# Performance work log

Hardware: AMD Instinct MI355X
Metric: run time of the kernel (lower is better)

## Reference

```python
import jax, jax.numpy as jnp
import numpy as np

HIDDEN = 2048
NUM_HEADS = 8
NUM_KV_HEADS = 1
HEAD_DIM = 256
ROPE_THETA = 10000.0
B, S = 2, 2048


def setup_inputs() -> dict:
    key = jax.random.key(0)
    k1, k2, k3, k4, k5 = jax.random.split(key, 5)
    scale = 0.02
    hidden_states = jax.random.normal(k1, (B, S, HIDDEN), dtype=jnp.float32)
    Wq = jax.random.normal(k2, (HIDDEN, NUM_HEADS * HEAD_DIM), dtype=jnp.float32) * scale
    Wk = jax.random.normal(k3, (HIDDEN, NUM_KV_HEADS * HEAD_DIM), dtype=jnp.float32) * scale
    Wv = jax.random.normal(k4, (HIDDEN, NUM_KV_HEADS * HEAD_DIM), dtype=jnp.float32) * scale
    Wo = jax.random.normal(k5, (NUM_HEADS * HEAD_DIM, HIDDEN), dtype=jnp.float32) * scale
    # causal mask: 1 = attend, 0 = masked (module adds -1e9 where mask==0)
    attention_mask = jnp.tril(jnp.ones((S, S), dtype=jnp.int32))[None, None].repeat(B, axis=0)
    position_ids = jnp.arange(S, dtype=jnp.int32)[None, :].repeat(B, axis=0)
    return {"hidden_states": hidden_states, "Wq": Wq, "Wk": Wk, "Wv": Wv,
            "Wo": Wo, "attention_mask": attention_mask, "position_ids": position_ids}


def _rotate_half(x):
    half = x.shape[-1] // 2
    return jnp.concatenate([-x[..., half:], x[..., :half]], axis=-1)


def _rope_cos_sin(position_ids, head_dim, theta):
    inv_freq = 1.0 / (theta ** (jnp.arange(0, head_dim, 2, dtype=jnp.float32) / head_dim))
    freqs = position_ids.astype(jnp.float32)[:, :, None] * inv_freq[None, None, :]  # [B,S,D/2]
    emb = jnp.concatenate([freqs, freqs], axis=-1)  # [B,S,D]
    return jnp.cos(emb)[:, None], jnp.sin(emb)[:, None]  # [B,1,S,D]


def reference(hidden_states, Wq, Wk, Wv, Wo, attention_mask, position_ids):
    bsz, q_len, _ = hidden_states.shape
    q = (hidden_states @ Wq).reshape(bsz, q_len, NUM_HEADS, HEAD_DIM).transpose(0, 2, 1, 3)
    k = (hidden_states @ Wk).reshape(bsz, q_len, NUM_KV_HEADS, HEAD_DIM).transpose(0, 2, 1, 3)
    v = (hidden_states @ Wv).reshape(bsz, q_len, NUM_KV_HEADS, HEAD_DIM).transpose(0, 2, 1, 3)
    q = q / jnp.sqrt(jnp.float32(HEAD_DIM))  # scale before RoPE, as in source
    cos, sin = _rope_cos_sin(position_ids, HEAD_DIM, ROPE_THETA)
    q = q * cos + _rotate_half(q) * sin
    k = k * cos + _rotate_half(k) * sin
    # GQA: repeat kv heads (prefill: cache == current k,v)
    groups = NUM_HEADS // NUM_KV_HEADS
    k = jnp.repeat(k, groups, axis=1)
    v = jnp.repeat(v, groups, axis=1)
    attn = jnp.einsum('bhqd,bhkd->bhqk', q, k)  # [B,H,S,S]
    additive = jnp.where(attention_mask == 0, jnp.float32(-1e9), jnp.float32(0.0))
    attn = jax.nn.softmax(attn + additive, axis=-1)
    out = jnp.einsum('bhqk,bhkd->bhqd', attn, v)
    out = out.transpose(0, 2, 1, 3).reshape(bsz, q_len, NUM_HEADS * HEAD_DIM)
    out = out @ Wo
    return out, attn
```

## Files before the change

kernel.cpp:

```cpp
#include <hip/hip_runtime.h>

typedef __bf16 bf16_t;
typedef __attribute__((ext_vector_type(4))) float f32x4;
typedef __attribute__((ext_vector_type(8))) __bf16 bf16x8;
typedef __attribute__((ext_vector_type(4))) __bf16 bf16x4;

#define DEVI __device__ __forceinline__

static constexpr int kBsz = 2, kS = 2048, kH = 8, kD = 256, kHid = 2048, kNqkv = 2560;

DEVI void gload_lds16(const void* g, void* l) {
  __builtin_amdgcn_global_load_lds(
      (__attribute__((address_space(1))) unsigned int*)g,
      (__attribute__((address_space(3))) unsigned int*)l, 16, 0, 0);
}

__global__ __launch_bounds__(256) void cast_f32_bf16(const float* __restrict__ in,
                                                     bf16_t* __restrict__ out) {
  int idx = blockIdx.x * 256 + threadIdx.x;
  const float4 f = ((const float4*)in)[idx];
  bf16x4 o;
  o[0] = (bf16_t)f.x; o[1] = (bf16_t)f.y; o[2] = (bf16_t)f.z; o[3] = (bf16_t)f.w;
  ((bf16x4*)out)[idx] = o;
}

__global__ __launch_bounds__(256) void zero_f32(float* __restrict__ p) {
  p[blockIdx.x * 256 + threadIdx.x] = 0.f;
}

__global__ void wtrans_all(const float* __restrict__ Wq, const float* __restrict__ Wk,
                           const float* __restrict__ Wv, const float* __restrict__ Wo,
                           bf16_t* __restrict__ WqkvT, bf16_t* __restrict__ WoT) {
  __shared__ float tile[32][33];
  int zb = blockIdx.x;
  const float* src;
  bf16_t* dst;
  int C, bx, by;
  if (zb < 4096) {
    src = Wq; dst = WqkvT; C = 2048; bx = zb & 63; by = zb >> 6;
  } else if (zb < 4608) {
    int u = zb - 4096; src = Wk; dst = WqkvT + (size_t)2048 * 2048; C = 256; bx = u & 7; by = u >> 3;
  } else if (zb < 5120) {
    int u = zb - 4608; src = Wv; dst = WqkvT + (size_t)2304 * 2048; C = 256; bx = u & 7; by = u >> 3;
  } else {
    int u = zb - 5120; src = Wo; dst = WoT; C = 2048; bx = u & 63; by = u >> 6;
  }
  int c0 = bx * 32, r0 = by * 32;
  int tx = threadIdx.x, ty = threadIdx.y;
#pragma unroll
  for (int k = 0; k < 4; k++)
    tile[ty + 8 * k][tx] = src[(size_t)(r0 + ty + 8 * k) * C + c0 + tx];
  __syncthreads();
#pragma unroll
  for (int k = 0; k < 4; k++)
    dst[(size_t)(c0 + ty + 8 * k) * 2048 + r0 + tx] = (bf16_t)tile[tx][ty + 8 * k];
}

__global__ __launch_bounds__(256) void transpose_v(const bf16_t* __restrict__ qkv,
                                                   bf16_t* __restrict__ vT) {
  __shared__ float tile[32][33];
  int d0 = blockIdx.x * 32, s0 = blockIdx.y * 32, b = blockIdx.z;
  int tx = threadIdx.x, ty = threadIdx.y;
  const bf16_t* in = qkv + ((size_t)(b * kS + s0)) * kNqkv + 2304 + d0;
#pragma unroll
  for (int k = 0; k < 4; k++)
    tile[ty + 8 * k][tx] = (float)in[(size_t)(ty + 8 * k) * kNqkv + tx];
  __syncthreads();
  bf16_t* out = vT + ((size_t)(b * kD + d0)) * kS + s0;
#pragma unroll
  for (int k = 0; k < 4; k++)
    out[(size_t)(ty + 8 * k) * kS + tx] = (bf16_t)tile[tx][ty + 8 * k];
}

__global__ __launch_bounds__(256) void rope_all(const bf16_t* __restrict__ qkv,
                                                const int* __restrict__ pos_ids,
                                                bf16_t* __restrict__ q_bh,
                                                bf16_t* __restrict__ k_b) {
  int bid = blockIdx.x;
  if (bid < 16384) {
    int idx = bid * 256 + threadIdx.x;
    int j = idx & 127, s = (idx >> 7) & 2047, h = (idx >> 18) & 7, b = idx >> 21;
    float invf = exp2f(-0.103810253f * (float)j);
    float ang = (float)pos_ids[b * kS + s] * invf;
    float c, sn;
    sincosf(ang, &sn, &c);
    const bf16_t* src = qkv + ((size_t)(b * kS + s)) * kNqkv + h * kD;
    float x0 = (float)src[j] * 0.0625f;
    float x1 = (float)src[j + 128] * 0.0625f;
    bf16_t* dst = q_bh + ((size_t)((b * kH + h) * kS + s)) * kD;
    dst[j] = (bf16_t)(x0 * c - x1 * sn);
    dst[j + 128] = (bf16_t)(x1 * c + x0 * sn);
  } else {
    int idx = (bid - 16384) * 256 + threadIdx.x;
    int j = idx & 127, s = (idx >> 7) & 2047, b = idx >> 18;
    float invf = exp2f(-0.103810253f * (float)j);
    float ang = (float)pos_ids[b * kS + s] * invf;
    float c, sn;
    sincosf(ang, &sn, &c);
    const bf16_t* src = qkv + ((size_t)(b * kS + s)) * kNqkv + 2048;
    float x0 = (float)src[j];
    float x1 = (float)src[j + 128];
    bf16_t* dst = k_b + ((size_t)(b * kS + s)) * kD;
    dst[j] = (bf16_t)(x0 * c - x1 * sn);
    dst[j + 128] = (bf16_t)(x1 * c + x0 * sn);
  }
}

__global__ __launch_bounds__(256, 4) void qk_exp(
    const bf16_t* __restrict__ q_bh, const bf16_t* __restrict__ k_b,
    bf16_t* __restrict__ P, float* __restrict__ rowsum) {
  __shared__ bf16_t ks[64 * 256];
  const int u = blockIdx.x;
  const int z = blockIdx.y;
  const int b = z >> 3;
  int rt = (int)((sqrtf(8.f * (float)u + 1.f) - 1.f) * 0.5f);
  while ((rt + 1) * (rt + 2) / 2 <= u) rt++;
  while (rt * (rt + 1) / 2 > u) rt--;
  const int kt = u - rt * (rt + 1) / 2;
  const int m0 = rt * 64, n0 = kt * 64;
  const int t = threadIdx.x, lane = t & 63, wv = t >> 6;
  const int wm2 = (wv & 1) * 32, wn2 = (wv >> 1) * 32;
  const int lrow = lane & 15, quad = lane >> 4;

  const bf16_t* kb = k_b + (size_t)b * kS * kD;
#pragma unroll
  for (int i = 0; i < 8; i++) {
    int slot = i * 256 + t;
    int r = slot >> 5;
    int c = (slot & 31) ^ (r & 7);
    gload_lds16(kb + (size_t)(n0 + r) * kD + c * 8, ks + slot * 8);
  }
  bf16x8 qf[2][8];
  {
    const bf16_t* qb = q_bh + ((size_t)z * kS + m0) * kD;
#pragma unroll
    for (int mi = 0; mi < 2; mi++)
#pragma unroll
      for (int k8 = 0; k8 < 8; k8++)
        qf[mi][k8] = *(const bf16x8*)(qb + (size_t)(wm2 + mi * 16 + lrow) * kD + k8 * 32 + quad * 8);
  }
  __syncthreads();

  f32x4 acc[2][2];
#pragma unroll
  for (int mi = 0; mi < 2; mi++)
#pragma unroll
    for (int ni = 0; ni < 2; ni++) acc[mi][ni] = f32x4{0.f, 0.f, 0.f, 0.f};
  __builtin_amdgcn_s_setprio(1);
#pragma unroll
  for (int k8 = 0; k8 < 8; k8++) {
    bf16x8 bfv[2];
#pragma unroll
    for (int ni = 0; ni < 2; ni++) {
      int R = wn2 + ni * 16 + lrow;
      int c16 = (k8 * 4 + quad) ^ (R & 7);
      bfv[ni] = *(const bf16x8*)(ks + R * 256 + c16 * 8);
    }
#pragma unroll
    for (int mi = 0; mi < 2; mi++)
#pragma unroll
      for (int ni = 0; ni < 2; ni++)
        acc[mi][ni] = __builtin_amdgcn_mfma_f32_16x16x32_bf16(qf[mi][k8], bfv[ni], acc[mi][ni], 0, 0, 0);
  }
  __builtin_amdgcn_s_setprio(0);

  const bool diag = (kt == rt);
  bf16_t* pt = P + ((size_t)z * kS + m0) * kS + n0;
#pragma unroll
  for (int mi = 0; mi < 2; mi++)
#pragma unroll
    for (int rr = 0; rr < 4; rr++) {
      int ml = wm2 + mi * 16 + quad * 4 + rr;
      int mg = m0 + ml;
      float s4 = 0.f;
#pragma unroll
      for (int ni = 0; ni < 2; ni++) {
        int nl = wn2 + ni * 16 + lrow;
        int ng = n0 + nl;
        float e = __expf(fminf(acc[mi][ni][rr], 80.f));
        bool ok = !diag || ng <= mg;
        bf16_t pb = ok ? (bf16_t)e : (bf16_t)0.f;
        pt[(size_t)ml * kS + nl] = pb;
        s4 += (float)pb;
      }
      s4 += __shfl_xor(s4, 1); s4 += __shfl_xor(s4, 2);
      s4 += __shfl_xor(s4, 4); s4 += __shfl_xor(s4, 8);
      if (lrow == 0) atomicAdd(rowsum + (size_t)z * kS + mg, s4);
    }

  if (diag && !(rt & 1)) {
    bf16x8 zz = {(bf16_t)0.f, (bf16_t)0.f, (bf16_t)0.f, (bf16_t)0.f,
                 (bf16_t)0.f, (bf16_t)0.f, (bf16_t)0.f, (bf16_t)0.f};
    int r = t >> 2, cc = (t & 3) * 16;
    bf16_t* pz = P + ((size_t)z * kS + m0 + r) * kS + n0 + 64 + cc;
    *(bf16x8*)pz = zz;
    *(bf16x8*)(pz + 8) = zz;
  }
}

__global__ __launch_bounds__(256) void attn_expand(
    const bf16_t* __restrict__ P, const float* __restrict__ rowsum,
    float* __restrict__ attn) {
  const int rt = blockIdx.y, z = blockIdx.z;
  const int m0 = rt * 64;
  const int t = threadIdx.x;
  const int r = t >> 2;
  const int cbase = blockIdx.x * 512 + (t & 3) * 8;
  const int ncaus = (rt + 1) * 64;
  const float inv = 1.f / rowsum[(size_t)z * kS + m0 + r];
  const size_t rowoff = ((size_t)z * kS + m0 + r) * kS;
  const bf16_t* pr = P + rowoff;
  float* ar = attn + rowoff;
#pragma unroll
  for (int it = 0; it < 16; it++) {
    int col = cbase + it * 32;
    float4 o0, o1;
    if (col < ncaus) {
      bf16x8 pv = *(const bf16x8*)(pr + col);
      o0 = make_float4((float)pv[0] * inv, (float)pv[1] * inv,
                       (float)pv[2] * inv, (float)pv[3] * inv);
      o1 = make_float4((float)pv[4] * inv, (float)pv[5] * inv,
                       (float)pv[6] * inv, (float)pv[7] * inv);
    } else {
      o0 = make_float4(0.f, 0.f, 0.f, 0.f);
      o1 = o0;
    }
    *(float4*)(ar + col) = o0;
    *(float4*)(ar + col + 4) = o1;
  }
}

template <int OUT, int CKTR, int BAL = 0>
__global__ __launch_bounds__(256) void gemm_bt(
    const bf16_t* __restrict__ Av, const bf16_t* __restrict__ Btv, void* __restrict__ Cv,
    int K, int lda, int ldb, int ldc,
    long long aBatch, long long bBatch, int bzShift, long long cBatch,
    const float* __restrict__ rowsum) {
  constexpr int BM = 128, BN = 128, BK = 64;
  __shared__ bf16_t As[BM * BK];
  __shared__ bf16_t Bs[BN * BK];
  const int z = blockIdx.z;
  const int n0 = blockIdx.x * BN;
  int byi = blockIdx.y;
  if (BAL) {
    if ((blockIdx.x ^ (blockIdx.z >> 3)) & 1) byi = gridDim.y - 1 - byi;
  }
  const int m0 = byi * BM;
  const bf16_t* Bt = Btv + (size_t)(z >> bzShift) * bBatch + (size_t)n0 * ldb;
  const int kEnd = CKTR ? ((m0 + BM < K) ? (m0 + BM) : K) : K;
  const int t = threadIdx.x;
  const int lane = t & 63, wv = t >> 6;
  const int wm = (wv & 1) << 6, wn = (wv >> 1) << 6;
  const int lrow = lane & 15, quad = lane >> 4;
  f32x4 zero = {0.f, 0.f, 0.f, 0.f};
  f32x4 acc[4][4];
#pragma unroll
  for (int i = 0; i < 4; i++)
#pragma unroll
    for (int j = 0; j < 4; j++) acc[i][j] = zero;

  const bf16_t* Ab = Av + (size_t)z * aBatch + (size_t)m0 * lda;

  for (int k0 = 0; k0 < kEnd; k0 += BK) {
    __syncthreads();
#pragma unroll
    for (int i = 0; i < 4; i++) {
      int slot = i * 256 + t;
      int r = slot >> 3, c = slot & 7;
      gload_lds16(Ab + (size_t)r * lda + k0 + c * 8, As + slot * 8);
    }
#pragma unroll
    for (int i = 0; i < 4; i++) {
      int slot = i * 256 + t;
      int r = slot >> 3, c = slot & 7;
      gload_lds16(Bt + (size_t)r * ldb + k0 + c * 8, Bs + slot * 8);
    }
    __syncthreads();
#pragma unroll
    for (int k8 = 0; k8 < 2; k8++) {
      bf16x8 af[4], bfv[4];
#pragma unroll
      for (int i = 0; i < 4; i++)
        af[i] = *(const bf16x8*)(As + (wm + i * 16 + lrow) * BK + k8 * 32 + quad * 8);
#pragma unroll
      for (int i = 0; i < 4; i++)
        bfv[i] = *(const bf16x8*)(Bs + (wn + i * 16 + lrow) * BK + k8 * 32 + quad * 8);
#pragma unroll
      for (int mi = 0; mi < 4; mi++)
#pragma unroll
        for (int ni = 0; ni < 4; ni++)
          acc[mi][ni] = __builtin_amdgcn_mfma_f32_16x16x32_bf16(af[mi], bfv[ni], acc[mi][ni], 0, 0, 0);
    }
  }

  if (OUT == 0) {
    float* C = (float*)Cv + (size_t)z * cBatch;
#pragma unroll
    for (int mi = 0; mi < 4; mi++) {
      int m = m0 + wm + mi * 16 + quad * 4;
#pragma unroll
      for (int ni = 0; ni < 4; ni++) {
        int n = n0 + wn + ni * 16 + lrow;
#pragma unroll
        for (int r = 0; r < 4; r++) C[(size_t)(m + r) * ldc + n] = acc[mi][ni][r];
      }
    }
  } else if (OUT == 1) {
    bf16_t* C = (bf16_t*)Cv + (size_t)(z >> 3) * cBatch + (size_t)(z & 7) * kD;
#pragma unroll
    for (int mi = 0; mi < 4; mi++) {
      int m = m0 + wm + mi * 16 + quad * 4;
      float inv[4];
#pragma unroll
      for (int r = 0; r < 4; r++) inv[r] = 1.f / rowsum[(size_t)z * kS + m + r];
#pragma unroll
      for (int ni = 0; ni < 4; ni++) {
        int n = n0 + wn + ni * 16 + lrow;
#pragma unroll
        for (int r = 0; r < 4; r++)
          C[(size_t)(m + r) * ldc + n] = (bf16_t)(acc[mi][ni][r] * inv[r]);
      }
    }
  } else {
    bf16_t* C = (bf16_t*)Cv + (size_t)z * cBatch;
#pragma unroll
    for (int mi = 0; mi < 4; mi++) {
      int m = m0 + wm + mi * 16 + quad * 4;
#pragma unroll
      for (int ni = 0; ni < 4; ni++) {
        int n = n0 + wn + ni * 16 + lrow;
#pragma unroll
        for (int r = 0; r < 4; r++) C[(size_t)(m + r) * ldc + n] = (bf16_t)acc[mi][ni][r];
      }
    }
  }
}

extern "C" void kernel_launch(void* const* d_in, const int* in_sizes, int n_in,
                              void* d_out, int out_size, void* d_ws, size_t ws_size,
                              hipStream_t stream) {
  const float* hs = (const float*)d_in[0];
  const float* Wq = (const float*)d_in[1];
  const float* Wk = (const float*)d_in[2];
  const float* Wv = (const float*)d_in[3];
  const float* Wo = (const float*)d_in[4];
  const int* pos = (const int*)d_in[6];

  float* out = (float*)d_out;
  float* attn = out + (size_t)kBsz * kS * kHid;

  char* w = (char*)d_ws;
  bf16_t* hsb = (bf16_t*)w;   w += (size_t)4096 * 2048 * 2;
  bf16_t* WqkvT = (bf16_t*)w; w += (size_t)2560 * 2048 * 2;
  bf16_t* WoT = (bf16_t*)w;   w += (size_t)2048 * 2048 * 2;
  bf16_t* qkv = (bf16_t*)w;   w += (size_t)4096 * 2560 * 2;
  bf16_t* q_bh = (bf16_t*)w;  w += (size_t)8388608 * 2;
  bf16_t* k_b = (bf16_t*)w;   w += (size_t)1048576 * 2;
  bf16_t* vT = (bf16_t*)w;    w += (size_t)1048576 * 2;
  bf16_t* av = (bf16_t*)w;    w += (size_t)8388608 * 2;
  bf16_t* Pb = (bf16_t*)w;    w += (size_t)16 * 2048 * 2048 * 2;
  float* rowsum = (float*)w;  w += (size_t)16 * 2048 * 4;

  cast_f32_bf16<<<8192, 256, 0, stream>>>(hs, hsb);
  wtrans_all<<<9216, dim3(32, 8), 0, stream>>>(Wq, Wk, Wv, Wo, WqkvT, WoT);
  zero_f32<<<128, 256, 0, stream>>>(rowsum);

  gemm_bt<2, 0><<<dim3(20, 32, 1), 256, 0, stream>>>(
      hsb, WqkvT, qkv, 2048, 2048, 2048, 2560, 0, 0, 0, 0, nullptr);

  rope_all<<<18432, 256, 0, stream>>>(qkv, pos, q_bh, k_b);
  transpose_v<<<dim3(8, 64, 2), dim3(32, 8), 0, stream>>>(qkv, vT);

  qk_exp<<<dim3(528, 16), 256, 0, stream>>>(q_bh, k_b, Pb, rowsum);

  attn_expand<<<dim3(4, 32, 16), 256, 0, stream>>>(Pb, rowsum, attn);

  gemm_bt<1, 1, 1><<<dim3(2, 16, 16), 256, 0, stream>>>(
      Pb, vT, av, 2048, 2048, 2048, 2048,
      (long long)4194304, (long long)524288, 3, (long long)(kS * kHid), rowsum);

  gemm_bt<0, 0><<<dim3(16, 32, 1), 256, 0, stream>>>(
      av, WoT, out, 2048, 2048, 2048, 2048, 0, 0, 0, 0, nullptr);
}
```

Baseline: 740.3 us.

## Merge prep and rope/transpose kernels; stage bf16 GEMM epilogue through LDS

Combines the cast, weight-transpose and rowsum-zero kernels into one launch, and the RoPE and V-transpose kernels into another, reducing launch count. The bf16-output GEMM epilogues now write the tile into swizzled shared memory and then emit coalesced 16-byte row stores instead of scattered 2-byte stores. This adds an extra LDS round trip and two barriers per tile, and puts divergent block roles in the merged kernels.

```diff
diff --git a/kernel.cpp b/kernel.cpp
--- a/kernel.cpp
+++ b/kernel.cpp
@@ -15,38 +15,42 @@
       (__attribute__((address_space(3))) unsigned int*)l, 16, 0, 0);
 }
 
-__global__ __launch_bounds__(256) void cast_f32_bf16(const float* __restrict__ in,
-                                                     bf16_t* __restrict__ out) {
-  int idx = blockIdx.x * 256 + threadIdx.x;
-  const float4 f = ((const float4*)in)[idx];
-  bf16x4 o;
-  o[0] = (bf16_t)f.x; o[1] = (bf16_t)f.y; o[2] = (bf16_t)f.z; o[3] = (bf16_t)f.w;
-  ((bf16x4*)out)[idx] = o;
-}
-
-__global__ __launch_bounds__(256) void zero_f32(float* __restrict__ p) {
-  p[blockIdx.x * 256 + threadIdx.x] = 0.f;
-}
-
-__global__ void wtrans_all(const float* __restrict__ Wq, const float* __restrict__ Wk,
-                           const float* __restrict__ Wv, const float* __restrict__ Wo,
-                           bf16_t* __restrict__ WqkvT, bf16_t* __restrict__ WoT) {
+__global__ __launch_bounds__(256) void prep_all(
+    const float* __restrict__ hs, const float* __restrict__ Wq,
+    const float* __restrict__ Wk, const float* __restrict__ Wv,
+    const float* __restrict__ Wo, bf16_t* __restrict__ hsb,
+    bf16_t* __restrict__ WqkvT, bf16_t* __restrict__ WoT,
+    float* __restrict__ rowsum) {
   __shared__ float tile[32][33];
-  int zb = blockIdx.x;
+  const int zb = blockIdx.x;
+  const int t = threadIdx.x;
+  if (zb < 8192) {
+    int idx = zb * 256 + t;
+    const float4 f = ((const float4*)hs)[idx];
+    bf16x4 o;
+    o[0] = (bf16_t)f.x; o[1] = (bf16_t)f.y; o[2] = (bf16_t)f.z; o[3] = (bf16_t)f.w;
+    ((bf16x4*)hsb)[idx] = o;
+    return;
+  }
+  if (zb >= 17408) {
+    rowsum[(zb - 17408) * 256 + t] = 0.f;
+    return;
+  }
+  const int u = zb - 8192;
   const float* src;
   bf16_t* dst;
   int C, bx, by;
-  if (zb < 4096) {
-    src = Wq; dst = WqkvT; C = 2048; bx = zb & 63; by = zb >> 6;
-  } else if (zb < 4608) {
-    int u = zb - 4096; src = Wk; dst = WqkvT + (size_t)2048 * 2048; C = 256; bx = u & 7; by = u >> 3;
-  } else if (zb < 5120) {
-    int u = zb - 4608; src = Wv; dst = WqkvT + (size_t)2304 * 2048; C = 256; bx = u & 7; by = u >> 3;
+  if (u < 4096) {
+    src = Wq; dst = WqkvT; C = 2048; bx = u & 63; by = u >> 6;
+  } else if (u < 4608) {
+    int v = u - 4096; src = Wk; dst = WqkvT + (size_t)2048 * 2048; C = 256; bx = v & 7; by = v >> 3;
+  } else if (u < 5120) {
+    int v = u - 4608; src = Wv; dst = WqkvT + (size_t)2304 * 2048; C = 256; bx = v & 7; by = v >> 3;
   } else {
-    int u = zb - 5120; src = Wo; dst = WoT; C = 2048; bx = u & 63; by = u >> 6;
+    int v = u - 5120; src = Wo; dst = WoT; C = 2048; bx = v & 63; by = v >> 6;
   }
   int c0 = bx * 32, r0 = by * 32;
-  int tx = threadIdx.x, ty = threadIdx.y;
+  int tx = t & 31, ty = t >> 5;
 #pragma unroll
   for (int k = 0; k < 4; k++)
     tile[ty + 8 * k][tx] = src[(size_t)(r0 + ty + 8 * k) * C + c0 + tx];
@@ -56,29 +60,16 @@
     dst[(size_t)(c0 + ty + 8 * k) * 2048 + r0 + tx] = (bf16_t)tile[tx][ty + 8 * k];
 }
 
-__global__ __launch_bounds__(256) void transpose_v(const bf16_t* __restrict__ qkv,
-                                                   bf16_t* __restrict__ vT) {
+__global__ __launch_bounds__(256) void rope_tv(const bf16_t* __restrict__ qkv,
+                                               const int* __restrict__ pos_ids,
+                                               bf16_t* __restrict__ q_bh,
+                                               bf16_t* __restrict__ k_b,
+                                               bf16_t* __restrict__ vT) {
   __shared__ float tile[32][33];
-  int d0 = blockIdx.x * 32, s0 = blockIdx.y * 32, b = blockIdx.z;
-  int tx = threadIdx.x, ty = threadIdx.y;
-  const bf16_t* in = qkv + ((size_t)(b * kS + s0)) * kNqkv + 2304 + d0;
-#pragma unroll
-  for (int k = 0; k < 4; k++)
-    tile[ty + 8 * k][tx] = (float)in[(size_t)(ty + 8 * k) * kNqkv + tx];
-  __syncthreads();
-  bf16_t* out = vT + ((size_t)(b * kD + d0)) * kS + s0;
-#pragma unroll
-  for (int k = 0; k < 4; k++)
-    out[(size_t)(ty + 8 * k) * kS + tx] = (bf16_t)tile[tx][ty + 8 * k];
-}
-
-__global__ __launch_bounds__(256) void rope_all(const bf16_t* __restrict__ qkv,
-                                                const int* __restrict__ pos_ids,
-                                                bf16_t* __restrict__ q_bh,
-                                                bf16_t* __restrict__ k_b) {
-  int bid = blockIdx.x;
+  const int bid = blockIdx.x;
+  const int t = threadIdx.x;
   if (bid < 16384) {
-    int idx = bid * 256 + threadIdx.x;
+    int idx = bid * 256 + t;
     int j = idx & 127, s = (idx >> 7) & 2047, h = (idx >> 18) & 7, b = idx >> 21;
     float invf = exp2f(-0.103810253f * (float)j);
     float ang = (float)pos_ids[b * kS + s] * invf;
@@ -90,8 +81,8 @@
     bf16_t* dst = q_bh + ((size_t)((b * kH + h) * kS + s)) * kD;
     dst[j] = (bf16_t)(x0 * c - x1 * sn);
     dst[j + 128] = (bf16_t)(x1 * c + x0 * sn);
-  } else {
-    int idx = (bid - 16384) * 256 + threadIdx.x;
+  } else if (bid < 18432) {
+    int idx = (bid - 16384) * 256 + t;
     int j = idx & 127, s = (idx >> 7) & 2047, b = idx >> 18;
     float invf = exp2f(-0.103810253f * (float)j);
     float ang = (float)pos_ids[b * kS + s] * invf;
@@ -103,6 +94,19 @@
     bf16_t* dst = k_b + ((size_t)(b * kS + s)) * kD;
     dst[j] = (bf16_t)(x0 * c - x1 * sn);
     dst[j + 128] = (bf16_t)(x1 * c + x0 * sn);
+  } else {
+    int u = bid - 18432;
+    int d0 = (u & 7) * 32, s0 = ((u >> 3) & 63) * 32, b = u >> 9;
+    int tx = t & 31, ty = t >> 5;
+    const bf16_t* in = qkv + ((size_t)(b * kS + s0)) * kNqkv + 2304 + d0;
+#pragma unroll
+    for (int k = 0; k < 4; k++)
+      tile[ty + 8 * k][tx] = (float)in[(size_t)(ty + 8 * k) * kNqkv + tx];
+    __syncthreads();
+    bf16_t* out = vT + ((size_t)(b * kD + d0)) * kS + s0;
+#pragma unroll
+    for (int k = 0; k < 4; k++)
+      out[(size_t)(ty + 8 * k) * kS + tx] = (bf16_t)tile[tx][ty + 8 * k];
   }
 }
 
@@ -237,8 +241,9 @@
     long long aBatch, long long bBatch, int bzShift, long long cBatch,
     const float* __restrict__ rowsum) {
   constexpr int BM = 128, BN = 128, BK = 64;
-  __shared__ bf16_t As[BM * BK];
-  __shared__ bf16_t Bs[BN * BK];
+  __shared__ bf16_t smem[BM * BK + BN * BK];
+  bf16_t* As = smem;
+  bf16_t* Bs = smem + BM * BK;
   const int z = blockIdx.z;
   const int n0 = blockIdx.x * BN;
   int byi = blockIdx.y;
@@ -305,33 +310,41 @@
         for (int r = 0; r < 4; r++) C[(size_t)(m + r) * ldc + n] = acc[mi][ni][r];
       }
     }
-  } else if (OUT == 1) {
-    bf16_t* C = (bf16_t*)Cv + (size_t)(z >> 3) * cBatch + (size_t)(z & 7) * kD;
+  } else {
+    __syncthreads();
 #pragma unroll
     for (int mi = 0; mi < 4; mi++) {
-      int m = m0 + wm + mi * 16 + quad * 4;
+      int mrow = wm + mi * 16 + quad * 4;
       float inv[4];
-#pragma unroll
-      for (int r = 0; r < 4; r++) inv[r] = 1.f / rowsum[(size_t)z * kS + m + r];
+      if (OUT == 1) {
+#pragma unroll
+        for (int r = 0; r < 4; r++)
+          inv[r] = 1.f / rowsum[(size_t)z * kS + m0 + mrow + r];
+      }
 #pragma unroll
       for (int ni = 0; ni < 4; ni++) {
-        int n = n0 + wn + ni * 16 + lrow;
-#pragma unroll
-        for (int r = 0; r < 4; r++)
-          C[(size_t)(m + r) * ldc + n] = (bf16_t)(acc[mi][ni][r] * inv[r]);
+        int ncol = wn + ni * 16 + lrow;
+#pragma unroll
+        for (int r = 0; r < 4; r++) {
+          int m_l = mrow + r;
+          int n_sw = ncol ^ ((m_l & 15) << 3);
+          float v = acc[mi][ni][r];
+          if (OUT == 1) v *= inv[r];
+          smem[m_l * BN + n_sw] = (bf16_t)v;
+        }
       }
     }
-  } else {
-    bf16_t* C = (bf16_t*)Cv + (size_t)z * cBatch;
-#pragma unroll
-    for (int mi = 0; mi < 4; mi++) {
-      int m = m0 + wm + mi * 16 + quad * 4;
-#pragma unroll
-      for (int ni = 0; ni < 4; ni++) {
-        int n = n0 + wn + ni * 16 + lrow;
-#pragma unroll
-        for (int r = 0; r < 4; r++) C[(size_t)(m + r) * ldc + n] = (bf16_t)acc[mi][ni][r];
-      }
+    __syncthreads();
+    bf16_t* Cb = (OUT == 1)
+        ? (bf16_t*)Cv + (size_t)(z >> 3) * cBatch + (size_t)(z & 7) * kD
+        : (bf16_t*)Cv + (size_t)z * cBatch;
+    int row = t >> 1, half = t & 1;
+#pragma unroll
+    for (int j = 0; j < 8; j++) {
+      int c0 = half * 64 + j * 8;
+      int c_sw = c0 ^ ((row & 15) << 3);
+      bf16x8 v = *(const bf16x8*)(smem + row * BN + c_sw);
+      *(bf16x8*)(Cb + (size_t)(m0 + row) * ldc + n0 + c0) = v;
     }
   }
 }
@@ -361,15 +374,12 @@
   bf16_t* Pb = (bf16_t*)w;    w += (size_t)16 * 2048 * 2048 * 2;
   float* rowsum = (float*)w;  w += (size_t)16 * 2048 * 4;
 
-  cast_f32_bf16<<<8192, 256, 0, stream>>>(hs, hsb);
-  wtrans_all<<<9216, dim3(32, 8), 0, stream>>>(Wq, Wk, Wv, Wo, WqkvT, WoT);
-  zero_f32<<<128, 256, 0, stream>>>(rowsum);
+  prep_all<<<17536, 256, 0, stream>>>(hs, Wq, Wk, Wv, Wo, hsb, WqkvT, WoT, rowsum);
 
   gemm_bt<2, 0><<<dim3(20, 32, 1), 256, 0, stream>>>(
       hsb, WqkvT, qkv, 2048, 2048, 2048, 2560, 0, 0, 0, 0, nullptr);
 
-  rope_all<<<18432, 256, 0, stream>>>(qkv, pos, q_bh, k_b);
-  transpose_v<<<dim3(8, 64, 2), dim3(32, 8), 0, stream>>>(qkv, vT);
+  rope_tv<<<19456, 256, 0, stream>>>(qkv, pos, q_bh, k_b, vT);
 
   qk_exp<<<dim3(528, 16), 256, 0, stream>>>(q_bh, k_b, Pb, rowsum);
 
```

After: 739.2 us. About the same (-0.1%).
